# Performance work log

Measured on AMD Instinct MI355X. Metric: run time of the kernel, lower is better.

## Reference

```python
import jax, jax.numpy as jnp
import numpy as np

HID = 4096      # hidden_size
H = 32          # num_attention_heads
K = 8           # num_key_value_heads
D = HID // H    # head_dim = 128
G = H // K      # q heads per kv group = 4
INTER = 14336   # intermediate_size
T = 2048        # tokens (prefill)
EPS = 1e-5
THETA = 1000000.0


def setup_inputs() -> dict:
    key = jax.random.key(0)
    ks = jax.random.split(key, 9)
    s = 0.02
    return {
        "hidden_states": jax.random.normal(ks[0], (T, HID), jnp.float32),
        "position_ids": jnp.arange(T, dtype=jnp.int64),
        "wqkv": jax.random.normal(ks[1], ((H + 2 * K) * D, HID), jnp.float32) * s,
        "wo": jax.random.normal(ks[2], (HID, HID), jnp.float32) * s,
        "w1": jax.random.normal(ks[3], (INTER, HID), jnp.float32) * s,  # gate
        "w3": jax.random.normal(ks[4], (INTER, HID), jnp.float32) * s,  # up
        "w2": jax.random.normal(ks[5], (HID, INTER), jnp.float32) * s,  # down
        "attn_norm_w": jnp.ones((HID,), jnp.float32),
        "ffn_norm_w": jnp.ones((HID,), jnp.float32),
    }


def _rmsnorm(x, w):
    var = jnp.mean(jnp.square(x), axis=-1, keepdims=True)
    return x * jax.lax.rsqrt(var + EPS) * w


def _rope(x, cos, sin):
    # non-interleaved (half-split) rotation; x: [T, h, D], cos/sin: [T, 1, D//2]
    x1, x2 = x[..., : D // 2], x[..., D // 2 :]
    return jnp.concatenate([x1 * cos - x2 * sin, x2 * cos + x1 * sin], axis=-1)


def _attention(x, position_ids, wqkv, wo):
    t = x.shape[0]
    qkv = x @ wqkv.T  # [T, (H+2K)*D]
    q = qkv[:, : H * D].reshape(t, H, D)
    k = qkv[:, H * D : (H + K) * D].reshape(t, K, D)
    v = qkv[:, (H + K) * D :].reshape(t, K, D)

    inv_freq = 1.0 / (THETA ** (jnp.arange(0, D, 2, dtype=jnp.float32) / D))
    freqs = position_ids.astype(jnp.float32)[:, None] * inv_freq  # [T, D//2]
    cos = jnp.cos(freqs)[:, None, :]
    sin = jnp.sin(freqs)[:, None, :]
    q = _rope(q, cos, sin)
    k = _rope(k, cos, sin)

    # grouped-query attention: [T, K, G, D] queries vs [T, K, D] keys
    qg = q.reshape(t, K, G, D)
    scale = 1.0 / jnp.sqrt(jnp.float32(D))
    scores = jnp.einsum("tkgd,skd->kgts", qg, k) * scale  # [K, G, T, T]
    causal = jnp.tril(jnp.ones((t, t), dtype=bool))
    scores = jnp.where(causal, scores, jnp.finfo(scores.dtype).min)
    probs = jax.nn.softmax(scores, axis=-1)
    out = jnp.einsum("kgts,skd->tkgd", probs, v).reshape(t, H * D)
    return out @ wo.T


def _mlp(x, w1, w3, w2):
    return (jax.nn.silu(x @ w1.T) * (x @ w3.T)) @ w2.T


def reference(hidden_states, position_ids, wqkv, wo, w1, w3, w2, attn_norm_w, ffn_norm_w):
    h = hidden_states + _attention(_rmsnorm(hidden_states, attn_norm_w), position_ids, wqkv, wo)
    return h + _mlp(_rmsnorm(h, ffn_norm_w), w1, w3, w2)
```

## Files before the change

kernel.cpp:

```cpp
#include <hip/hip_runtime.h>
#include <stdint.h>

#define T_SEQ 2048
#define HIDN  4096
#define NH    32
#define NKV   8
#define DH    128
#define INTER 14336
#define QKV_N 6144
#define EPSR  1e-5f
#define SCALE 0.08838834764831845f
#define KVB   64

typedef __bf16 bf16x8 __attribute__((ext_vector_type(8)));
typedef float  f32x4  __attribute__((ext_vector_type(4)));

__device__ __forceinline__ f32x4 mfma16(bf16x8 a, bf16x8 b, f32x4 c) {
  return __builtin_amdgcn_mfma_f32_16x16x32_bf16(a, b, c, 0, 0, 0);
}

__device__ __forceinline__ void glds16(const void* g, void* l) {
  __builtin_amdgcn_global_load_lds(
      (__attribute__((address_space(1))) void*)g,
      (__attribute__((address_space(3))) void*)l,
      16, 0, 0);
}

__global__ __launch_bounds__(256) void cvt_bf16_kernel(
    const float* __restrict__ src, __bf16* __restrict__ dst, long n) {
  long stride = (long)gridDim.x * 256 * 8;
  for (long i = ((long)blockIdx.x * 256 + threadIdx.x) * 8; i < n; i += stride) {
    float4 a = *(const float4*)(src + i);
    float4 b = *(const float4*)(src + i + 4);
    bf16x8 o;
    o[0]=(__bf16)a.x; o[1]=(__bf16)a.y; o[2]=(__bf16)a.z; o[3]=(__bf16)a.w;
    o[4]=(__bf16)b.x; o[5]=(__bf16)b.y; o[6]=(__bf16)b.z; o[7]=(__bf16)b.w;
    *(bf16x8*)(dst + i) = o;
  }
}

__global__ __launch_bounds__(256) void rmsnorm_kernel(
    const float* __restrict__ x, const float* __restrict__ w,
    __bf16* __restrict__ y) {
  const int row = blockIdx.x, tid = threadIdx.x;
  const float* xr = x + (size_t)row * HIDN + tid * 16;
  float4 v0 = ((const float4*)xr)[0];
  float4 v1 = ((const float4*)xr)[1];
  float4 v2 = ((const float4*)xr)[2];
  float4 v3 = ((const float4*)xr)[3];
  float ss = v0.x*v0.x + v0.y*v0.y + v0.z*v0.z + v0.w*v0.w
           + v1.x*v1.x + v1.y*v1.y + v1.z*v1.z + v1.w*v1.w
           + v2.x*v2.x + v2.y*v2.y + v2.z*v2.z + v2.w*v2.w
           + v3.x*v3.x + v3.y*v3.y + v3.z*v3.z + v3.w*v3.w;
  #pragma unroll
  for (int off = 32; off >= 1; off >>= 1) ss += __shfl_xor(ss, off, 64);
  __shared__ float red[4];
  if ((tid & 63) == 0) red[tid >> 6] = ss;
  __syncthreads();
  float rn = rsqrtf((red[0] + red[1] + red[2] + red[3]) * (1.0f / HIDN) + EPSR);
  const float* wr = w + tid * 16;
  float4 w0 = ((const float4*)wr)[0];
  float4 w1v = ((const float4*)wr)[1];
  float4 w2v = ((const float4*)wr)[2];
  float4 w3v = ((const float4*)wr)[3];
  bf16x8 o0, o1;
  o0[0]=(__bf16)(v0.x*rn*w0.x);  o0[1]=(__bf16)(v0.y*rn*w0.y);
  o0[2]=(__bf16)(v0.z*rn*w0.z);  o0[3]=(__bf16)(v0.w*rn*w0.w);
  o0[4]=(__bf16)(v1.x*rn*w1v.x); o0[5]=(__bf16)(v1.y*rn*w1v.y);
  o0[6]=(__bf16)(v1.z*rn*w1v.z); o0[7]=(__bf16)(v1.w*rn*w1v.w);
  o1[0]=(__bf16)(v2.x*rn*w2v.x); o1[1]=(__bf16)(v2.y*rn*w2v.y);
  o1[2]=(__bf16)(v2.z*rn*w2v.z); o1[3]=(__bf16)(v2.w*rn*w2v.w);
  o1[4]=(__bf16)(v3.x*rn*w3v.x); o1[5]=(__bf16)(v3.y*rn*w3v.y);
  o1[6]=(__bf16)(v3.z*rn*w3v.z); o1[7]=(__bf16)(v3.w*rn*w3v.w);
  __bf16* yo = y + (size_t)row * HIDN + tid * 16;
  *(bf16x8*)(yo)     = o0;
  *(bf16x8*)(yo + 8) = o1;
}

template<int EPI>
__global__ __launch_bounds__(512, 2) void gemm256_kernel(
    const __bf16* __restrict__ A, const __bf16* __restrict__ B,
    void* __restrict__ Cout, int M, int N, int Kfull, int KZ) {
  extern __shared__ __align__(16) char smem[];
  const int tid = threadIdx.x;
  const int lane = tid & 63;
  const int wv = tid >> 6;
  const int wm = wv >> 2;
  const int wn = wv & 3;
  const int lr = lane & 15, q = lane >> 4;

  const int gx = gridDim.x, gy = gridDim.y;
  const int nwg = gx * gy;
  const int orig = blockIdx.y * gx + blockIdx.x;
  const int cpx = nwg >> 3;
  const int swz = (orig & 7) * cpx + (orig >> 3);
  const int by = swz % gy, bx = swz / gy;
  const int m0 = by * 256, n0 = bx * 256;
  const int kbase = blockIdx.z * KZ;
  const int NT = KZ >> 5;

  const char* aS[2]; const char* bS[2]; int Lds[2];
  #pragma unroll
  for (int j = 0; j < 2; j++) {
    int L = j * 512 + tid;
    int row = L >> 2;
    int s = (L & 3) ^ ((row >> 1) & 3);
    aS[j] = (const char*)(A + (size_t)(m0 + row) * Kfull + kbase + s * 8);
    bS[j] = (const char*)(B + (size_t)(n0 + row) * Kfull + kbase + s * 8);
    Lds[j] = L * 16;
  }

  const int sA = q ^ ((lr >> 1) & 3);
  int aoff[8], boff[4];
  #pragma unroll
  for (int mt = 0; mt < 8; mt++) aoff[mt] = (wm * 128 + mt * 16 + lr) * 64 + sA * 16;
  #pragma unroll
  for (int nt = 0; nt < 4; nt++) boff[nt] = 16384 + (wn * 64 + nt * 16 + lr) * 64 + sA * 16;

#define STAGE_T(tile, sb) do {                                   \
    char* _b = smem + (sb) * 32768;                              \
    size_t _ko = (size_t)(tile) * 64;                            \
    glds16(aS[0] + _ko, _b + Lds[0]);                            \
    glds16(aS[1] + _ko, _b + Lds[1]);                            \
    glds16(bS[0] + _ko, _b + 16384 + Lds[0]);                    \
    glds16(bS[1] + _ko, _b + 16384 + Lds[1]);                    \
  } while (0)

#define GBODY(VMC, DOST) do {                                    \
    if (DOST) { STAGE_T(t + 3, sbufi); sbufi = (sbufi == 4) ? 0 : sbufi + 1; } \
    asm volatile("s_waitcnt vmcnt(" #VMC ")" ::: "memory");      \
    __builtin_amdgcn_s_barrier();                                \
    asm volatile("" ::: "memory");                               \
    __builtin_amdgcn_sched_barrier(0);                           \
    { const char* _bA = smem + bufi * 32768;                     \
      bf16x8 bf[4], af[8];                                       \
      _Pragma("unroll") for (int nt = 0; nt < 4; nt++)           \
        bf[nt] = *(const bf16x8*)(_bA + boff[nt]);               \
      _Pragma("unroll") for (int mt = 0; mt < 8; mt++)           \
        af[mt] = *(const bf16x8*)(_bA + aoff[mt]);               \
      __builtin_amdgcn_s_setprio(1);                             \
      _Pragma("unroll") for (int mt = 0; mt < 8; mt++)           \
        _Pragma("unroll") for (int nt = 0; nt < 4; nt++)         \
          acc[mt][nt] = mfma16(af[mt], bf[nt], acc[mt][nt]);     \
      __builtin_amdgcn_s_setprio(0); }                           \
    bufi = (bufi == 4) ? 0 : bufi + 1;                           \
  } while (0)

  f32x4 acc[8][4] = {};
  STAGE_T(0, 0); STAGE_T(1, 1); STAGE_T(2, 2);
  int bufi = 0, sbufi = 3;
  for (int t = 0; t < NT - 3; ++t) GBODY(12, true);
  { int t = 0; (void)t;
    GBODY(8, false); GBODY(4, false); GBODY(0, false); }
#undef STAGE_T
#undef GBODY

  #pragma unroll
  for (int mt = 0; mt < 8; mt++) {
    #pragma unroll
    for (int r = 0; r < 4; r++) {
      int rr = m0 + wm * 128 + mt * 16 + q * 4 + r;
      #pragma unroll
      for (int nt = 0; nt < 4; nt++) {
        int cc = n0 + wn * 64 + nt * 16 + lr;
        size_t ix = (size_t)rr * N + cc;
        float val = acc[mt][nt][r];
        if (EPI == 0) ((float*)Cout)[(size_t)blockIdx.z * M * N + ix] = val;
        else          ((__bf16*)Cout)[ix] = (__bf16)val;
      }
    }
  }
}

__global__ __launch_bounds__(256) void add3_kernel(
    const float* __restrict__ p, const float* __restrict__ r,
    float* __restrict__ o, long n) {
  long stride = (long)gridDim.x * 1024;
  for (long i = ((long)blockIdx.x * 256 + threadIdx.x) * 4; i < n; i += stride) {
    float4 a = *(const float4*)(p + i);
    float4 b = *(const float4*)(p + n + i);
    float4 c = *(const float4*)(r + i);
    float4 o4;
    o4.x = a.x + b.x + c.x; o4.y = a.y + b.y + c.y;
    o4.z = a.z + b.z + c.z; o4.w = a.w + b.w + c.w;
    *(float4*)(o + i) = o4;
  }
}

__global__ __launch_bounds__(256) void rope_kernel(
    const __bf16* __restrict__ qkv, __bf16* __restrict__ q_r,
    __bf16* __restrict__ k_r) {
  const int t = blockIdx.x, tid = threadIdx.x;
  __shared__ float cs[64], sn[64];
  if (tid < 64) {
    float inv = exp2f(-(float)tid * (19.931568569324174f / 64.0f));
    float f = (float)t * inv;
    cs[tid] = cosf(f);
    sn[tid] = sinf(f);
  }
  __syncthreads();
  const __bf16* row = qkv + (size_t)t * QKV_N;
  for (int it = tid; it < 40 * 64; it += 256) {
    int hh = it >> 6, i = it & 63;
    float x1 = (float)row[hh * 128 + i];
    float x2 = (float)row[hh * 128 + 64 + i];
    float c = cs[i], s = sn[i];
    float o1 = x1 * c - x2 * s;
    float o2 = x2 * c + x1 * s;
    if (hh < NH) {
      __bf16* qo = q_r + (size_t)t * HIDN + hh * 128;
      qo[i] = (__bf16)o1;
      qo[64 + i] = (__bf16)o2;
    } else {
      __bf16* ko = k_r + (size_t)t * (NKV * DH) + (hh - NH) * 128;
      ko[i] = (__bf16)o1;
      ko[64 + i] = (__bf16)o2;
    }
  }
}

__global__ __launch_bounds__(256) void vtrans_kernel(
    const __bf16* __restrict__ qkv, __bf16* __restrict__ v_t) {
  __shared__ __bf16 tile[64][136];
  const int tid = threadIdx.x;
  const int t0 = blockIdx.x * 64, kh = blockIdx.y;
  #pragma unroll
  for (int i = 0; i < 4; i++) {
    int u = i * 256 + tid;
    int row = u >> 4, c = (u & 15) * 8;
    *(bf16x8*)&tile[row][c] =
        *(const bf16x8*)(qkv + (size_t)(t0 + row) * QKV_N + (NH + NKV) * DH + kh * DH + c);
  }
  __syncthreads();
  const int d = tid & 127, th = (tid >> 7) * 32;
  #pragma unroll
  for (int j = 0; j < 4; j++) {
    int t = th + j * 8;
    bf16x8 o;
    #pragma unroll
    for (int e = 0; e < 8; e++) o[e] = tile[t + e][d];
    *(bf16x8*)(v_t + ((size_t)kh * DH + d) * T_SEQ + t0 + t) = o;
  }
}

__global__ __launch_bounds__(256) void attn_kernel(
    const __bf16* __restrict__ q_r, const __bf16* __restrict__ k_r,
    const __bf16* __restrict__ v_t, __bf16* __restrict__ attn_o) {
  __shared__ __align__(16) __bf16 Ks[KVB * 128];
  __shared__ __align__(16) __bf16 Vs[128 * KVB];
  __shared__ __align__(16) __bf16 Pl[4 * 16 * KVB];

  const int tid = threadIdx.x;
  const int lane = tid & 63, wv = tid >> 6;
  const int lr = lane & 15, g = lane >> 4;
  const int qt = gridDim.x - 1 - blockIdx.x;
  const int h = blockIdx.y;
  const int kh = h >> 2;
  const int q0b = qt * 64;
  const int q0w = q0b + wv * 16;

  bf16x8 qf[4];
  {
    const __bf16* qp = q_r + (size_t)(q0w + lr) * HIDN + h * DH + g * 8;
    #pragma unroll
    for (int kk = 0; kk < 4; kk++) qf[kk] = *(const bf16x8*)(qp + kk * 32);
  }

  f32x4 o[8] = {};
  float mrun[4] = {-1e30f, -1e30f, -1e30f, -1e30f};
  float lrun[4] = {0.f, 0.f, 0.f, 0.f};
  char* PlW = (char*)Pl + wv * 2048;

  for (int kv0 = 0; kv0 < q0b + KVB; kv0 += KVB) {
    __syncthreads();
    #pragma unroll
    for (int i = 0; i < 4; i++) {
      int u = i * 256 + tid;
      int row = u >> 4;
      int cb = ((u & 15) * 16) ^ ((row & 7) << 4);
      glds16((const char*)(k_r + (size_t)(kv0 + row) * (NKV * DH) + kh * DH) + cb,
             (char*)Ks + u * 16);
    }
    #pragma unroll
    for (int i = 0; i < 4; i++) {
      int u = i * 256 + tid;
      int row = u >> 3;
      int cb = ((u & 7) * 16) ^ ((row & 7) << 4);
      glds16((const char*)(v_t + ((size_t)kh * DH + row) * T_SEQ + kv0) + cb,
             (char*)Vs + u * 16);
    }
    __syncthreads();

    if (q0w + 15 >= kv0) {
      f32x4 s[4] = {};
      #pragma unroll
      for (int kk = 0; kk < 4; kk++) {
        #pragma unroll
        for (int jt = 0; jt < 4; jt++) {
          int krow = jt * 16 + lr;
          int cb = (kk * 64 + g * 16) ^ ((krow & 7) << 4);
          bf16x8 kf = *(const bf16x8*)((char*)Ks + krow * 256 + cb);
          s[jt] = mfma16(qf[kk], kf, s[jt]);
        }
      }
      const bool need_mask = (kv0 + KVB - 1) > q0w;
      #pragma unroll
      for (int r = 0; r < 4; r++) {
        int qpos = q0w + g * 4 + r;
        int prow = g * 4 + r;
        float p[4];
        #pragma unroll
        for (int jt = 0; jt < 4; jt++) {
          float v = s[jt][r] * SCALE;
          if (need_mask && (kv0 + jt * 16 + lr > qpos)) v = -1e30f;
          p[jt] = v;
        }
        float mx = fmaxf(fmaxf(p[0], p[1]), fmaxf(p[2], p[3]));
        #pragma unroll
        for (int off = 1; off < 16; off <<= 1) mx = fmaxf(mx, __shfl_xor(mx, off, 64));
        float mn = fmaxf(mrun[r], mx);
        float corr = __expf(mrun[r] - mn);
        mrun[r] = mn;
        float ps = 0.f;
        #pragma unroll
        for (int jt = 0; jt < 4; jt++) {
          p[jt] = __expf(p[jt] - mn);
          ps += p[jt];
          int cbyte = ((jt * 16 + lr) * 2) ^ ((prow & 7) << 4);
          *(__bf16*)(PlW + prow * 128 + cbyte) = (__bf16)p[jt];
        }
        #pragma unroll
        for (int off = 1; off < 16; off <<= 1) ps += __shfl_xor(ps, off, 64);
        lrun[r] = lrun[r] * corr + ps;
        #pragma unroll
        for (int nt = 0; nt < 8; nt++) o[nt][r] *= corr;
      }
      bf16x8 pa[2];
      #pragma unroll
      for (int ks = 0; ks < 2; ks++)
        pa[ks] = *(const bf16x8*)(PlW + lr * 128 + ((g * 16 + ks * 64) ^ ((lr & 7) << 4)));
      #pragma unroll
      for (int nt = 0; nt < 8; nt++) {
        #pragma unroll
        for (int ks = 0; ks < 2; ks++) {
          int vrow = nt * 16 + lr;
          int cb = (ks * 64 + g * 16) ^ ((vrow & 7) << 4);
          bf16x8 vf = *(const bf16x8*)((char*)Vs + vrow * 128 + cb);
          o[nt] = mfma16(pa[ks], vf, o[nt]);
        }
      }
    }
  }

  #pragma unroll
  for (int nt = 0; nt < 8; nt++) {
    #pragma unroll
    for (int r = 0; r < 4; r++) {
      int qrow = q0w + g * 4 + r;
      int d = nt * 16 + lr;
      attn_o[(size_t)qrow * HIDN + h * DH + d] = (__bf16)(o[nt][r] / lrun[r]);
    }
  }
}

__global__ __launch_bounds__(256) void silu_mul_kernel(
    const __bf16* __restrict__ u, const __bf16* __restrict__ v,
    __bf16* __restrict__ g, long n) {
  long stride = (long)gridDim.x * 256 * 8;
  for (long i = ((long)blockIdx.x * 256 + threadIdx.x) * 8; i < n; i += stride) {
    bf16x8 uu = *(const bf16x8*)(u + i);
    bf16x8 vv = *(const bf16x8*)(v + i);
    bf16x8 gg;
    #pragma unroll
    for (int j = 0; j < 8; j++) {
      float x = (float)uu[j];
      float y = (float)vv[j];
      float sl = x / (1.0f + __expf(-x));
      gg[j] = (__bf16)(sl * y);
    }
    *(bf16x8*)(g + i) = gg;
  }
}

extern "C" void kernel_launch(void* const* d_in, const int* in_sizes, int n_in,
                              void* d_out, int out_size, void* d_ws, size_t ws_size,
                              hipStream_t stream) {
  const float* hidden = (const float*)d_in[0];
  const float* wqkv = (const float*)d_in[2];
  const float* wo   = (const float*)d_in[3];
  const float* w1   = (const float*)d_in[4];
  const float* w3   = (const float*)d_in[5];
  const float* w2   = (const float*)d_in[6];
  const float* anw  = (const float*)d_in[7];
  const float* fnw  = (const float*)d_in[8];

  char* ws = (char*)d_ws;
  const size_t SZ_XN   = (size_t)T_SEQ * HIDN * 2;
  const size_t SZ_QKV  = (size_t)T_SEQ * QKV_N * 2;
  const size_t SZ_KR   = (size_t)T_SEQ * NKV * DH * 2;
  const size_t SZ_H    = (size_t)T_SEQ * HIDN * 4;
  const size_t SZ_UV   = (size_t)T_SEQ * INTER * 2;

  const size_t W_QKV = (size_t)QKV_N * HIDN * 2;
  const size_t W_O   = (size_t)HIDN * HIDN * 2;
  const size_t W_I   = (size_t)INTER * HIDN * 2;
  const size_t W_TOTAL = W_QKV + W_O + 3 * W_I;

  char* act = ws + W_TOTAL;

  __bf16* xn1    = (__bf16*)(act);
  __bf16* qkv    = (__bf16*)(act + SZ_XN);
  __bf16* q_r    = (__bf16*)(act + SZ_XN + SZ_QKV);
  __bf16* ubuf   = (__bf16*)(act);
  __bf16* k_r    = (__bf16*)(act + SZ_UV);
  __bf16* attn_o = (__bf16*)(act + SZ_UV + SZ_KR);
  float*  hbuf   = (float*) (act + SZ_UV + SZ_KR + SZ_XN);
  __bf16* v_t    = (__bf16*)(act + SZ_UV + SZ_KR + SZ_XN);
  __bf16* xn2    = (__bf16*)(act + SZ_UV + SZ_KR + SZ_XN + SZ_H);
  __bf16* vbuf   = (__bf16*)(act + SZ_UV + SZ_KR + SZ_XN + SZ_H + SZ_XN);
  __bf16* gbuf   = ubuf;
  float*  pbuf   = (float*)(act + SZ_UV + SZ_KR + SZ_XN + SZ_H);

  __bf16* wqkv_b = (__bf16*)(ws);
  __bf16* wo_b   = (__bf16*)(ws + W_QKV);
  __bf16* w1_b   = (__bf16*)(ws + W_QKV + W_O);
  __bf16* w3_b   = (__bf16*)(ws + W_QKV + W_O + W_I);
  __bf16* w2_b   = (__bf16*)(ws + W_QKV + W_O + 2 * W_I);

  const int LDS_BYTES = 163840;
  hipFuncSetAttribute((const void*)gemm256_kernel<0>,
                      hipFuncAttributeMaxDynamicSharedMemorySize, LDS_BYTES);
  hipFuncSetAttribute((const void*)gemm256_kernel<1>,
                      hipFuncAttributeMaxDynamicSharedMemorySize, LDS_BYTES);

  cvt_bf16_kernel<<<2048, 256, 0, stream>>>(wqkv, wqkv_b, (long)QKV_N * HIDN);
  cvt_bf16_kernel<<<2048, 256, 0, stream>>>(wo,   wo_b,   (long)HIDN * HIDN);
  cvt_bf16_kernel<<<2048, 256, 0, stream>>>(w1,   w1_b,   (long)INTER * HIDN);
  cvt_bf16_kernel<<<2048, 256, 0, stream>>>(w3,   w3_b,   (long)INTER * HIDN);
  cvt_bf16_kernel<<<2048, 256, 0, stream>>>(w2,   w2_b,   (long)HIDN * INTER);

  rmsnorm_kernel<<<T_SEQ, 256, 0, stream>>>(hidden, anw, xn1);
  gemm256_kernel<1><<<dim3(QKV_N / 256, T_SEQ / 256, 1), 512, LDS_BYTES, stream>>>(
      xn1, wqkv_b, qkv, T_SEQ, QKV_N, HIDN, HIDN);
  rope_kernel<<<T_SEQ, 256, 0, stream>>>(qkv, q_r, k_r);
  vtrans_kernel<<<dim3(T_SEQ / 64, NKV), 256, 0, stream>>>(qkv, v_t);
  attn_kernel<<<dim3(T_SEQ / 64, NH), 256, 0, stream>>>(q_r, k_r, v_t, attn_o);
  gemm256_kernel<0><<<dim3(HIDN / 256, T_SEQ / 256, 2), 512, LDS_BYTES, stream>>>(
      attn_o, wo_b, pbuf, T_SEQ, HIDN, HIDN, HIDN / 2);
  add3_kernel<<<2048, 256, 0, stream>>>(pbuf, hidden, hbuf, (long)T_SEQ * HIDN);
  rmsnorm_kernel<<<T_SEQ, 256, 0, stream>>>(hbuf, fnw, xn2);
  gemm256_kernel<1><<<dim3(INTER / 256, T_SEQ / 256, 1), 512, LDS_BYTES, stream>>>(
      xn2, w1_b, ubuf, T_SEQ, INTER, HIDN, HIDN);
  gemm256_kernel<1><<<dim3(INTER / 256, T_SEQ / 256, 1), 512, LDS_BYTES, stream>>>(
      xn2, w3_b, vbuf, T_SEQ, INTER, HIDN, HIDN);
  silu_mul_kernel<<<2048, 256, 0, stream>>>(ubuf, vbuf, gbuf, (long)T_SEQ * INTER);
  gemm256_kernel<0><<<dim3(HIDN / 256, T_SEQ / 256, 2), 512, LDS_BYTES, stream>>>(
      gbuf, w2_b, pbuf, T_SEQ, HIDN, INTER, INTER / 2);
  add3_kernel<<<2048, 256, 0, stream>>>(pbuf, hbuf, (float*)d_out, (long)T_SEQ * HIDN);
}
```

Measured before the change: 1.342 ms.

## Restructure GEMM main loop into double-buffered 64-K tiles with split fine-grained staging

Replaces the 5-stage 32-K ring buffer in the 256x256 GEMM with a 2-buffer scheme of 64-K tiles split into two 32-K halves. Global-to-LDS loads for A and B halves are interleaved between half-tile MFMA groups, each fenced by barriers and lgkmcnt waits. The goal is finer interleaving of memory traffic with MFMA work and a smaller LDS footprint. In exchange it adds many more barriers per tile and a shallower prefetch depth, which could expose load latency.

```diff
diff --git a/kernel.cpp b/kernel.cpp
--- a/kernel.cpp
+++ b/kernel.cpp
@@ -87,7 +87,7 @@
   const int wv = tid >> 6;
   const int wm = wv >> 2;
   const int wn = wv & 3;
-  const int lr = lane & 15, q = lane >> 4;
+  const int lr = lane & 15, ql = lane >> 4;
 
   const int gx = gridDim.x, gy = gridDim.y;
   const int nwg = gx * gy;
@@ -97,69 +97,116 @@
   const int by = swz % gy, bx = swz / gy;
   const int m0 = by * 256, n0 = bx * 256;
   const int kbase = blockIdx.z * KZ;
-  const int NT = KZ >> 5;
-
-  const char* aS[2]; const char* bS[2]; int Lds[2];
-  #pragma unroll
-  for (int j = 0; j < 2; j++) {
-    int L = j * 512 + tid;
-    int row = L >> 2;
-    int s = (L & 3) ^ ((row >> 1) & 3);
-    aS[j] = (const char*)(A + (size_t)(m0 + row) * Kfull + kbase + s * 8);
-    bS[j] = (const char*)(B + (size_t)(n0 + row) * Kfull + kbase + s * 8);
-    Lds[j] = L * 16;
-  }
-
-  const int sA = q ^ ((lr >> 1) & 3);
+  const int NT = KZ >> 6;
+
+  const int u0 = tid, u1 = tid + 512;
+  const int r0 = u0 >> 2, r1 = u1 >> 2;
+  const int p0 = (u0 & 3) ^ ((r0 >> 1) & 3);
+  const int p1 = (u1 & 3) ^ ((r1 >> 1) & 3);
+  const char* aR0 = (const char*)(A + (size_t)(m0 + r0) * Kfull + kbase) + p0 * 16;
+  const char* aR1 = (const char*)(A + (size_t)(m0 + r1) * Kfull + kbase) + p1 * 16;
+  const char* bR0 = (const char*)(B + (size_t)(n0 + r0) * Kfull + kbase) + p0 * 16;
+  const char* bR1 = (const char*)(B + (size_t)(n0 + r1) * Kfull + kbase) + p1 * 16;
+  const int d0 = u0 * 16, d1 = u1 * 16;
+
+  const int sA = ql ^ ((lr >> 1) & 3);
   int aoff[8], boff[4];
   #pragma unroll
   for (int mt = 0; mt < 8; mt++) aoff[mt] = (wm * 128 + mt * 16 + lr) * 64 + sA * 16;
   #pragma unroll
-  for (int nt = 0; nt < 4; nt++) boff[nt] = 16384 + (wn * 64 + nt * 16 + lr) * 64 + sA * 16;
-
-#define STAGE_T(tile, sb) do {                                   \
-    char* _b = smem + (sb) * 32768;                              \
-    size_t _ko = (size_t)(tile) * 64;                            \
-    glds16(aS[0] + _ko, _b + Lds[0]);                            \
-    glds16(aS[1] + _ko, _b + Lds[1]);                            \
-    glds16(bS[0] + _ko, _b + 16384 + Lds[0]);                    \
-    glds16(bS[1] + _ko, _b + 16384 + Lds[1]);                    \
+  for (int nt = 0; nt < 4; nt++) boff[nt] = (wn * 64 + nt * 16 + lr) * 64 + sA * 16;
+
+#define STAGE_A(t, kh, b) do {                                         \
+    const size_t _o = (size_t)(t) * 128 + (kh) * 64;                   \
+    glds16(aR0 + _o, smem + (b) * 65536 + (kh) * 16384 + d0);          \
+    glds16(aR1 + _o, smem + (b) * 65536 + (kh) * 16384 + d1);          \
   } while (0)
-
-#define GBODY(VMC, DOST) do {                                    \
-    if (DOST) { STAGE_T(t + 3, sbufi); sbufi = (sbufi == 4) ? 0 : sbufi + 1; } \
-    asm volatile("s_waitcnt vmcnt(" #VMC ")" ::: "memory");      \
-    __builtin_amdgcn_s_barrier();                                \
-    asm volatile("" ::: "memory");                               \
-    __builtin_amdgcn_sched_barrier(0);                           \
-    { const char* _bA = smem + bufi * 32768;                     \
-      bf16x8 bf[4], af[8];                                       \
-      _Pragma("unroll") for (int nt = 0; nt < 4; nt++)           \
-        bf[nt] = *(const bf16x8*)(_bA + boff[nt]);               \
-      _Pragma("unroll") for (int mt = 0; mt < 8; mt++)           \
-        af[mt] = *(const bf16x8*)(_bA + aoff[mt]);               \
-      __builtin_amdgcn_s_setprio(1);                             \
-      _Pragma("unroll") for (int mt = 0; mt < 8; mt++)           \
-        _Pragma("unroll") for (int nt = 0; nt < 4; nt++)         \
-          acc[mt][nt] = mfma16(af[mt], bf[nt], acc[mt][nt]);     \
-      __builtin_amdgcn_s_setprio(0); }                           \
-    bufi = (bufi == 4) ? 0 : bufi + 1;                           \
+#define STAGE_B(t, kh, b) do {                                         \
+    const size_t _o = (size_t)(t) * 128 + (kh) * 64;                   \
+    glds16(bR0 + _o, smem + (b) * 65536 + 32768 + (kh) * 16384 + d0);  \
+    glds16(bR1 + _o, smem + (b) * 65536 + 32768 + (kh) * 16384 + d1);  \
   } while (0)
+#define LDA4(dst, mb, b, ks) do {                                      \
+    const char* _p = smem + (b) * 65536 + (ks) * 16384;                \
+    dst[0] = *(const bf16x8*)(_p + aoff[(mb) + 0]);                    \
+    dst[1] = *(const bf16x8*)(_p + aoff[(mb) + 1]);                    \
+    dst[2] = *(const bf16x8*)(_p + aoff[(mb) + 2]);                    \
+    dst[3] = *(const bf16x8*)(_p + aoff[(mb) + 3]);                    \
+  } while (0)
+#define LDB4(b, ks) do {                                               \
+    const char* _p = smem + (b) * 65536 + 32768 + (ks) * 16384;        \
+    bfr[0] = *(const bf16x8*)(_p + boff[0]);                           \
+    bfr[1] = *(const bf16x8*)(_p + boff[1]);                           \
+    bfr[2] = *(const bf16x8*)(_p + boff[2]);                           \
+    bfr[3] = *(const bf16x8*)(_p + boff[3]);                           \
+  } while (0)
+#define VMW8() asm volatile("s_waitcnt vmcnt(8)" ::: "memory")
+#define BAR()  __builtin_amdgcn_s_barrier()
+#define WAITK() do { asm volatile("s_waitcnt lgkmcnt(0)" ::: "memory"); \
+    __builtin_amdgcn_sched_barrier(0); } while (0)
+#define MFMA16(mb, AF) do {                                            \
+    __builtin_amdgcn_s_setprio(1);                                     \
+    _Pragma("unroll") for (int _m = 0; _m < 4; _m++)                   \
+      _Pragma("unroll") for (int _n = 0; _n < 4; _n++)                 \
+        acc[(mb) + _m][_n] = mfma16(AF[_m], bfr[_n], acc[(mb) + _m][_n]); \
+    __builtin_amdgcn_s_setprio(0);                                     \
+  } while (0)
 
   f32x4 acc[8][4] = {};
-  STAGE_T(0, 0); STAGE_T(1, 1); STAGE_T(2, 2);
-  int bufi = 0, sbufi = 3;
-  for (int t = 0; t < NT - 3; ++t) GBODY(12, true);
-  { int t = 0; (void)t;
-    GBODY(8, false); GBODY(4, false); GBODY(0, false); }
-#undef STAGE_T
-#undef GBODY
+  bf16x8 afA[4], afB[4], bfr[4];
+
+  STAGE_A(0, 0, 0); STAGE_B(0, 0, 0);
+  STAGE_A(0, 1, 0); STAGE_B(0, 1, 0);
+  STAGE_A(1, 0, 1); STAGE_B(1, 0, 1);
+  VMW8();
+  BAR();
+
+  const int NI = NT >> 1;
+  for (int i = 0; i < NI; ++i) {
+    const int t1 = 2 * i + 1;
+    const int s2 = (2 * i + 2 < NT) ? 2 * i + 2 : NT - 1;
+    const int s3 = (2 * i + 3 < NT) ? 2 * i + 3 : NT - 1;
+    LDA4(afA, 0, 0, 0); LDB4(0, 0);
+    STAGE_A(t1, 1, 1);
+    BAR(); WAITK(); MFMA16(0, afA); BAR();
+    LDA4(afB, 4, 0, 0);
+    STAGE_B(t1, 1, 1);
+    VMW8(); BAR(); WAITK(); MFMA16(4, afB); BAR();
+    LDA4(afA, 0, 0, 1); LDB4(0, 1);
+    STAGE_A(s2, 0, 0);
+    BAR(); WAITK(); MFMA16(0, afA); BAR();
+    LDA4(afB, 4, 0, 1);
+    STAGE_B(s2, 0, 0);
+    VMW8(); BAR(); WAITK(); MFMA16(4, afB); BAR();
+    LDA4(afA, 0, 1, 0); LDB4(1, 0);
+    STAGE_A(s2, 1, 0);
+    BAR(); WAITK(); MFMA16(0, afA); BAR();
+    LDA4(afB, 4, 1, 0);
+    STAGE_B(s2, 1, 0);
+    VMW8(); BAR(); WAITK(); MFMA16(4, afB); BAR();
+    LDA4(afA, 0, 1, 1); LDB4(1, 1);
+    STAGE_A(s3, 0, 1);
+    BAR(); WAITK(); MFMA16(0, afA); BAR();
+    LDA4(afB, 4, 1, 1);
+    STAGE_B(s3, 0, 1);
+    VMW8(); BAR(); WAITK(); MFMA16(4, afB); BAR();
+  }
+  asm volatile("s_waitcnt vmcnt(0)" ::: "memory");
+
+#undef STAGE_A
+#undef STAGE_B
+#undef LDA4
+#undef LDB4
+#undef VMW8
+#undef BAR
+#undef WAITK
+#undef MFMA16
 
   #pragma unroll
   for (int mt = 0; mt < 8; mt++) {
     #pragma unroll
     for (int r = 0; r < 4; r++) {
-      int rr = m0 + wm * 128 + mt * 16 + q * 4 + r;
+      int rr = m0 + wm * 128 + mt * 16 + ql * 4 + r;
       #pragma unroll
       for (int nt = 0; nt < 4; nt++) {
         int cc = n0 + wn * 64 + nt * 16 + lr;
@@ -427,7 +474,7 @@
   __bf16* w3_b   = (__bf16*)(ws + W_QKV + W_O + W_I);
   __bf16* w2_b   = (__bf16*)(ws + W_QKV + W_O + 2 * W_I);
 
-  const int LDS_BYTES = 163840;
+  const int LDS_BYTES = 131072;
   hipFuncSetAttribute((const void*)gemm256_kernel<0>,
                       hipFuncAttributeMaxDynamicSharedMemorySize, LDS_BYTES);
   hipFuncSetAttribute((const void*)gemm256_kernel<1>,
```

Measured after the change: 1.326 ms. Within noise of the previous version (-1.2%).
